# Kernel tuning notes

Hardware: AMD Instinct MI355X
Metric: run time of the kernel (lower is better)

Reference implementation:

```python
import jax, jax.numpy as jnp
import numpy as np

G = 64          # number of global tokens (first G positions are global)
NUM_HEADS = 16
WINDOW = 512    # attention_window (one-sided w = 256)


def _chunk(x, w):
    # x: [BH, S, D] -> overlapping chunks of size 2w with overlap w
    BH, S, D = x.shape
    f = x.reshape(BH, S // w, w, D)
    return jnp.concatenate([f[:, :-1], f[:, 1:]], axis=2)  # [BH, S//w-1, 2w, D]


def _mask_invalid(x, w):
    # x: [B, S, H, 2w+1]; -inf at out-of-sequence window positions
    B, S, H, W = x.shape
    m = jnp.flip(jnp.tril(jnp.ones((w, w + 1), x.dtype)), axis=0)
    m = jnp.pad(m, ((0, S - w), (0, W - w - 1)))
    m = m + jnp.flip(m, axis=(0, 1))
    return jnp.where((m > 0)[None, :, None, :], -jnp.inf, x)


def _sliding_qk(q, k, w):
    # q, k: [B, S, H, D] -> banded scores [B, S, H, 2w+1]
    B, S, H, D = q.shape
    C = S // w - 1
    qf = q.transpose(0, 2, 1, 3).reshape(B * H, S, D)
    kf = k.transpose(0, 2, 1, 3).reshape(B * H, S, D)
    s = jnp.einsum('bcxd,bcyd->bcxy', _chunk(qf, w), _chunk(kf, w))  # [BH,C,2w,2w]
    diag = jnp.pad(s, ((0, 0), (0, 0), (0, 1), (0, 0))).transpose(0, 1, 3, 2)  # [BH,C,2w,2w+1]
    up = jnp.concatenate([diag[:, :, :w, :w + 1], diag[:, -1:, w:, :w + 1]], axis=1)
    z = jnp.zeros((B * H, 1, w, w), diag.dtype)
    low = jnp.concatenate([z, diag[:, :, -(w + 1):-1, w + 1:]], axis=1)
    first = jnp.concatenate([jnp.roll(diag, shift=(1, w), axis=(2, 3))[:, :, :w, :w], z], axis=1)
    low = jnp.where(jnp.arange(C + 1)[None, :, None, None] < 1, first, low)
    full = jnp.concatenate([low, up], axis=-1).reshape(B, H, S, 2 * w + 1).transpose(0, 2, 1, 3)
    return _mask_invalid(full, w)


def _sliding_pv(probs, v, w):
    # probs: [B, S, H, 2w+1], v: [B, S, H, D] -> [B, S, H, D]
    B, S, H, _ = probs.shape
    D = v.shape[-1]
    nc = S // w
    p = probs.transpose(0, 2, 1, 3).reshape(B * H, nc, w, 2 * w + 1)
    vf = v.transpose(0, 2, 1, 3).reshape(B * H, S, D)
    pv = jnp.pad(vf, ((0, 0), (w, w), (0, 0)), constant_values=-1.0)
    idx = jnp.arange(nc)[:, None] * w + jnp.arange(3 * w)[None, :]
    cv = pv[:, idx]  # [BH, nc, 3w, D]
    # pad-and-diagonalize the banded probs into [w, 3w]
    pd = jnp.pad(p, ((0, 0), (0, 0), (0, 0), (0, w + 1)))
    pd = pd.reshape(B * H, nc, w * (3 * w + 2))[:, :, :-w]
    pd = pd.reshape(B * H, nc, w, 3 * w + 1)[:, :, :, :-1]  # [BH,nc,w,3w]
    out = jnp.einsum('bcwd,bcdh->bcwh', pd, cv)
    return out.reshape(B, H, S, D).transpose(0, 2, 1, 3)


def _forward(hidden_states, attention_mask, Wq, bq, Wk, bk, Wv, bv,
             Wqg, bqg, Wkg, bkg, Wvg, bvg, is_index_masked, is_index_global_attn):
    B, S, E = hidden_states.shape
    H = NUM_HEADS
    D = E // H
    w = WINDOW // 2
    q = (hidden_states @ Wq + bq) / jnp.sqrt(jnp.float32(D))
    k = hidden_states @ Wk + bk
    v = hidden_states @ Wv + bv
    q4 = q.reshape(B, S, H, D)
    k4 = k.reshape(B, S, H, D)
    v4 = v.reshape(B, S, H, D)
    local = _sliding_qk(q4, k4, w)                         # [B,S,H,2w+1]
    diag_mask = _sliding_qk(jnp.ones_like(attention_mask), attention_mask, w)  # [B,S,1,2w+1]
    local = local + diag_mask
    # global key columns (first G tokens global) prepended to the band
    g_scores = jnp.einsum('bshd,bghd->bshg', q4, k4[:, :G])
    scores = jnp.concatenate([g_scores, local], axis=-1)   # [B,S,H,G+2w+1]
    probs = jax.nn.softmax(scores, axis=-1)
    probs = jnp.where(is_index_masked[:, :, None, None], 0.0, probs)
    out_g = jnp.einsum('bshg,bghd->bshd', probs[..., :G], v4[:, :G])
    out_l = _sliding_pv(probs[..., G:], v4, w)
    attn_output = (out_g + out_l).reshape(B, S, E)
    # global tokens attend to the full sequence with the *_global projections
    qg = ((hidden_states[:, :G] @ Wqg + bqg) / jnp.sqrt(jnp.float32(D))).reshape(B, G, H, D).transpose(0, 2, 1, 3)
    kg = (hidden_states @ Wkg + bkg).reshape(B, S, H, D).transpose(0, 2, 1, 3)
    vg = (hidden_states @ Wvg + bvg).reshape(B, S, H, D).transpose(0, 2, 1, 3)
    gs = jnp.einsum('bhgd,bhsd->bhgs', qg, kg)             # [B,H,G,S]
    gs = jnp.where(is_index_masked[:, None, None, :], -10000.0, gs)
    gp = jax.nn.softmax(gs, axis=-1)
    go = jnp.einsum('bhgs,bhsd->bhgd', gp, vg).transpose(0, 2, 1, 3).reshape(B, G, E)
    attn_output = attn_output.at[:, :G].set(go)            # scatter global rows
    probs = jnp.where(is_index_global_attn[:, :, None, None], 0.0, probs)
    return attn_output, probs, gp


def setup_inputs() -> dict:
    key = jax.random.key(0)
    B, S, E = 2, 4096, 1024
    ks = jax.random.split(key, 8)
    std = 0.02
    d = lambda k: std * jax.random.normal(k, (E, E), jnp.float32)
    zb = jnp.zeros((E,), jnp.float32)
    return {
        'hidden_states': jax.random.normal(ks[0], (B, S, E), jnp.float32),
        'attention_mask': jnp.zeros((B, S, 1, 1), jnp.float32),
        'Wq': d(ks[1]), 'bq': zb, 'Wk': d(ks[2]), 'bk': zb, 'Wv': d(ks[3]), 'bv': zb,
        'Wqg': d(ks[4]), 'bqg': zb, 'Wkg': d(ks[5]), 'bkg': zb, 'Wvg': d(ks[6]), 'bvg': zb,
        'is_index_masked': jnp.zeros((B, S), bool),
        'is_index_global_attn': jnp.broadcast_to(jnp.arange(S)[None, :] < G, (B, S)),
        'is_global_attn': 1,
    }


def reference(hidden_states, attention_mask, Wq, bq, Wk, bk, Wv, bv,
              Wqg, bqg, Wkg, bkg, Wvg, bvg,
              is_index_masked, is_index_global_attn, is_global_attn):
    # is_global_attn is statically 1 (global path always taken)
    return _forward(hidden_states, attention_mask, Wq, bq, Wk, bk, Wv, bv,
                    Wqg, bqg, Wkg, bkg, Wvg, bvg, is_index_masked, is_index_global_attn)
```

## Files before the change

### kernel.cpp

```cpp
#include <hip/hip_runtime.h>
#include <hip/hip_bf16.h>
#include <cstdint>
#include <cstddef>

typedef short s16x8 __attribute__((ext_vector_type(8)));
typedef float f32x4 __attribute__((ext_vector_type(4)));

#define DEV static __device__ __forceinline__

DEV unsigned short f2bf(float x){
  union { float f; unsigned int u; } v; v.f = x;
  unsigned int u = v.u;
  return (unsigned short)((u + 0x7FFFu + ((u >> 16) & 1u)) >> 16);
}
DEV float bf2f(unsigned short b){
  union { unsigned int u; float f; } v; v.u = ((unsigned int)b) << 16;
  return v.f;
}

DEV void gld16(unsigned short* lds, const unsigned short* g){
  __builtin_amdgcn_global_load_lds(
      (const __attribute__((address_space(1))) void*)g,
      (__attribute__((address_space(3))) void*)lds, 16, 0, 0);
}

__global__ __launch_bounds__(256) void cast_x(const float* __restrict__ X,
                                              unsigned short* __restrict__ out){
  int i = (blockIdx.x*256 + threadIdx.x)*4;
  float4 v = *(const float4*)(X + i);
  ushort4 r;
  r.x = f2bf(v.x); r.y = f2bf(v.y); r.z = f2bf(v.z); r.w = f2bf(v.w);
  *(ushort4*)(out + i) = r;
}

__global__ __launch_bounds__(256) void xg_gather(const float* __restrict__ X,
                                                 unsigned short* __restrict__ Xg){
  int idx = blockIdx.x*256 + threadIdx.x;
  int row = idx >> 10, c = idx & 1023;
  int b = row >> 6, g = row & 63;
  Xg[idx] = f2bf(X[(size_t)(b*4096 + g)*1024 + c]);
}

__global__ __launch_bounds__(256) void bias_cat_k(
    const float* bq, const float* bk, const float* bv,
    const float* bkg, const float* bvg, const float* bqg,
    float* __restrict__ bc, float* __restrict__ bqg_o){
  int i = blockIdx.x*256 + threadIdx.x;
  if (i < 5120){
    int slot = i >> 10, c = i & 1023;
    const float* s = (slot==0)?bq:(slot==1)?bk:(slot==2)?bv:(slot==3)?bkg:bvg;
    bc[i] = s[c];
  } else {
    bqg_o[i-5120] = bqg[i-5120];
  }
}

struct WSrc { const float* p[6]; };

__global__ __launch_bounds__(256) void wt_transpose(WSrc srcs,
    unsigned short* __restrict__ Wtcat, unsigned short* __restrict__ Wtqg){
  __shared__ float t[64*66];
  int bi = blockIdx.x;
  int widx = bi >> 8;
  int tile = bi & 255;
  int tn = tile & 15, tk = tile >> 4;
  int k0 = tk*64, n0 = tn*64;
  const float* W = srcs.p[widx];
  int tid = threadIdx.x;
  for (int it=0; it<8; ++it){
    int flat = it*256 + tid;
    int r = flat >> 5, ch = flat & 31;
    *(float2*)&t[r*66 + ch*2] = *(const float2*)(W + (size_t)(k0+r)*1024 + n0 + ch*2);
  }
  __syncthreads();
  unsigned short* dst = (widx==3) ? Wtqg
                      : Wtcat + (size_t)((widx<3)?widx:widx-1)*1048576;
  for (int it=0; it<16; ++it){
    int flat = it*256 + tid;
    int i = flat >> 6, j = flat & 63;
    dst[(size_t)(n0+i)*1024 + k0 + j] = f2bf(t[j*66 + i]);
  }
}

__global__ __launch_bounds__(256) void gemm_bt(
    const unsigned short* __restrict__ A, const unsigned short* __restrict__ Bt,
    const float* __restrict__ bias, unsigned short* __restrict__ C,
    int Astr, int Bstr, int Cstr, int scale_cols)
{
  __shared__ unsigned short lA[128*64];
  __shared__ unsigned short lB[128*64];
  int tid = threadIdx.x, lane = tid & 63, wv = tid >> 6;
  int wm = wv >> 1, wn = wv & 1;
  int lane15 = lane & 15, kh = (lane >> 4) << 3;
  int m0 = blockIdx.y*128, n0 = blockIdx.x*128;
  f32x4 acc[4][4];
  for (int i=0;i<4;i++) for (int j=0;j<4;j++) acc[i][j] = (f32x4){0.f,0.f,0.f,0.f};
  for (int k0 = 0; k0 < 1024; k0 += 64){
#pragma unroll
    for (int it = 0; it < 4; ++it){
      int chunk = it*256 + tid;
      int r = chunk >> 3, ch = chunk & 7;
      int co = ((ch ^ (r & 7)) << 3);
      gld16(&lA[chunk*8], A  + (size_t)(m0+r)*Astr + k0 + co);
      gld16(&lB[chunk*8], Bt + (size_t)(n0+r)*Bstr + k0 + co);
    }
    __syncthreads();
#pragma unroll
    for (int ks = 0; ks < 2; ++ks){
      s16x8 af[4], bfr[4];
#pragma unroll
      for (int i=0;i<4;i++){
        int row = wm*64 + i*16 + lane15;
        af[i] = *(const s16x8*)&lA[(row<<6) + ((ks*32 + kh) ^ ((row&7)<<3))];
      }
#pragma unroll
      for (int j=0;j<4;j++){
        int row = wn*64 + j*16 + lane15;
        bfr[j] = *(const s16x8*)&lB[(row<<6) + ((ks*32 + kh) ^ ((row&7)<<3))];
      }
#pragma unroll
      for (int i=0;i<4;i++)
#pragma unroll
        for (int j=0;j<4;j++)
          acc[i][j] = __builtin_amdgcn_mfma_f32_16x16x32_bf16(af[i], bfr[j], acc[i][j], 0,0,0);
    }
    __syncthreads();
  }
  for (int i=0;i<4;i++){
    int mb = m0 + wm*64 + i*16 + ((lane>>4)<<2);
    for (int j=0;j<4;j++){
      int n = n0 + wn*64 + j*16 + lane15;
      float bb = bias[n];
      float sc = (n < scale_cols) ? 0.125f : 1.0f;
#pragma unroll
      for (int r=0;r<4;r++)
        C[(size_t)(mb+r)*Cstr + n] = f2bf((acc[i][j][r] + bb)*sc);
    }
  }
}

__global__ __launch_bounds__(256) void vt_transpose(
    const unsigned short* __restrict__ proj, unsigned short* __restrict__ dst,
    int coloff){
  __shared__ unsigned short t[64*72];
  int bi = blockIdx.x;
  int sc = bi & 63, h = (bi>>6) & 15, b = bi >> 10;
  int s0 = sc*64;
  int tid = threadIdx.x;
  for (int it=0; it<2; ++it){
    int flat = it*256 + tid;
    int r = flat >> 3, ch = flat & 7;
    *(int4*)&t[r*72 + ch*8] =
      *(const int4*)(proj + (size_t)(b*4096+s0+r)*5120 + coloff + h*64 + ch*8);
  }
  __syncthreads();
  for (int it=0; it<2; ++it){
    int flat = it*256 + tid;
    int d = flat & 63, ch = flat >> 6;
    unsigned short tmp[8];
#pragma unroll
    for (int j=0;j<8;j++) tmp[j] = t[(ch*8+j)*72 + d];
    *(int4*)(dst + ((size_t)(b*16+h)*64 + d)*4096 + s0 + ch*8) = *(int4*)tmp;
  }
}

#define SSTR 612
__global__ __launch_bounds__(512) void sliding_attn(
    const unsigned short* __restrict__ proj,
    const unsigned short* __restrict__ vt,
    const float* __restrict__ amask,
    const unsigned char* __restrict__ maskb,
    float* __restrict__ probs,
    float* __restrict__ attn)
{
  __shared__ float sS[16*SSTR];
  __shared__ float srs[16];
  int bi = (blockIdx.x & 7)*1024 + (blockIdx.x >> 3);
  int ti = bi & 255, h = (bi>>8) & 15, b = bi >> 12;
  int t = ti*16;
  int chk = t >> 8;
  int qu = (chk < 15) ? chk*256 : 3584;
  int ql = (chk >= 1) ? chk*256 : 256;
  int tid = threadIdx.x, lane = tid & 63, wv = tid >> 6;
  int lane15 = lane & 15, kh = (lane >> 4) << 3;
  int rbase = (lane>>4)<<2;

  s16x8 aq0 = {}, aq1 = {}, ak0a = {}, ak0b = {}, ak1a = {}, ak1b = {};
  {
    int qrow = t + lane15;
    if (wv == 0){
      const unsigned short* qp = proj + (size_t)(b*4096+qrow)*5120 + h*64 + kh;
      aq0 = *(const s16x8*)qp;  aq1 = *(const s16x8*)(qp + 32);
    }
    if (wv >= 4){
      const unsigned short* kp0 = proj + (size_t)(b*4096+qrow)*5120 + 1024 + h*64 + kh;
      ak0a = *(const s16x8*)kp0; ak0b = *(const s16x8*)(kp0 + 32);
    }
    if (wv <= 3){
      int krow = t - 1 + lane15; if (krow < 0) krow = 0;
      const unsigned short* kp1 = proj + (size_t)(b*4096+krow)*5120 + 1024 + h*64 + kh;
      ak1a = *(const s16x8*)kp1; ak1b = *(const s16x8*)(kp1 + 32);
    }
  }

  {
    int ct0 = wv*5;
#pragma unroll
    for (int b2 = 0; b2 < 2; ++b2){
      const int nb = b2 ? 2 : 3;
      int cbase = ct0 + (b2 ? 3 : 0);
      s16x8 B0[3], B1[3];
#pragma unroll
      for (int j = 0; j < nb; ++j){
        int ct = cbase + j;
        if (ct < 37){
          int col = ct*16 + lane15;
          int brow, roff;
          if (ct < 4){        brow = col;               roff = 1024; }
          else if (ct < 20){  brow = ql + 1 + col - 64; roff = 0;
                              if (brow > 4095) brow = 4095; }
          else {              brow = qu + col - 320;    roff = 0; }
          const unsigned short* bp = proj + (size_t)(b*4096+brow)*5120 + roff + h*64 + kh;
          B0[j] = *(const s16x8*)bp;
          B1[j] = *(const s16x8*)(bp + 32);
        }
      }
#pragma unroll
      for (int j = 0; j < nb; ++j){
        int ct = cbase + j;
        if (ct < 37){
          s16x8 A0 = (ct<4) ? aq0 : (ct<20) ? ak1a : ak0a;
          s16x8 A1 = (ct<4) ? aq1 : (ct<20) ? ak1b : ak0b;
          f32x4 acc = (f32x4){0.f,0.f,0.f,0.f};
          acc = __builtin_amdgcn_mfma_f32_16x16x32_bf16(A0, B0[j], acc, 0,0,0);
          acc = __builtin_amdgcn_mfma_f32_16x16x32_bf16(A1, B1[j], acc, 0,0,0);
          int col = ct*16 + lane15;
          if (col <= 576){
            int sk = (ct >= 4);
#pragma unroll
            for (int r=0;r<4;r++){
              int row = rbase + r;
              sS[row*SSTR + col + (sk ? row : 0)] = acc[r];
            }
          }
        }
      }
    }
  }
  __syncthreads();

  {
    int r0 = wv*2;
    float low_add[2], up_add[2];
#pragma unroll
    for (int rr=0;rr<2;rr++){
      int s = t + r0 + rr;
      low_add[rr] = (s >= 1) ? amask[b*4096 + s - 1] : 0.f;
      up_add[rr]  = amask[b*4096 + s];
    }
    float ereg[2][10];
    float m4[2] = {-1e30f,-1e30f};
#pragma unroll
    for (int i=0;i<10;i++){
      int c = lane + i*64;
      bool inr = (c < 577);
      bool isup = (c >= 320), islow = (c >= 64) & !isup;
      int jup = c - 320, jlow = c - 64;
#pragma unroll
      for (int rr=0;rr<2;rr++){
        int r = r0 + rr;
        float v = -1e30f;
        if (inr){
          v = sS[r*SSTR + c + ((c>=64) ? r : 0)];
          int ii = (t + r) & 255;
          if (isup){
            bool valid = !((chk==15) & (jup >= 256 - ii));
            v = valid ? v + up_add[rr] : -1e30f;
          } else if (islow){
            bool valid = !((chk==0) & (jlow < 256 - ii));
            v = valid ? ((jlow==255) ? 0.f : v + low_add[rr]) : -1e30f;
          }
        }
        ereg[rr][i] = v;
        m4[rr] = fmaxf(m4[rr], v);
      }
    }
#pragma unroll
    for (int o=32;o;o>>=1){
#pragma unroll
      for (int rr=0;rr<2;rr++) m4[rr] = fmaxf(m4[rr], __shfl_xor(m4[rr], o));
    }
    float sum4[2] = {0.f,0.f};
#pragma unroll
    for (int i=0;i<10;i++){
      int c = lane + i*64;
      if (c < 577){
#pragma unroll
        for (int rr=0;rr<2;rr++){
          int r = r0 + rr;
          float e = __expf(ereg[rr][i] - m4[rr]);
          ereg[rr][i] = e;
          sum4[rr] += e;
          ((unsigned short*)&sS[r*SSTR])[c + ((c>=64) ? r : 0)] = f2bf(e);
        }
      }
    }
#pragma unroll
    for (int o=32;o;o>>=1){
#pragma unroll
      for (int rr=0;rr<2;rr++) sum4[rr] += __shfl_xor(sum4[rr], o);
    }
#pragma unroll
    for (int rr=0;rr<2;rr++){
      int r = r0 + rr, s = t + r;
      float rs = 1.f / sum4[rr];
      float mz = maskb[b*4096 + s] ? 0.f : 1.f;
      float pz = (s < 64) ? 0.f : mz;
      float* prow = probs + ((size_t)(b*4096+s)*16 + h)*577;
#pragma unroll
      for (int i=0;i<10;i++){
        int c = lane + i*64;
        if (c < 577) prow[c] = ereg[rr][i] * rs * pz;
      }
      if (lane < 31){
        int zc = (lane < r) ? 64 + lane : 577 + lane;
        ((unsigned short*)&sS[r*SSTR])[zc] = 0;
      }
      if (lane == 0) srs[r] = rs * mz;
    }
  }
  __syncthreads();

  int dg = wv & 3, khalf = wv >> 2;
  int dcol = dg*16 + lane15;
  const unsigned short* vtb = vt + ((size_t)(b*16+h)*64 + dcol)*4096;
  const unsigned short* prow16 = (const unsigned short*)(sS + (size_t)lane15*SSTR);
  f32x4 oacc = (f32x4){0.f,0.f,0.f,0.f};
  int kc0 = khalf*10, kcend = kc0 + (khalf ? 9 : 10);
#pragma unroll
  for (int b2 = 0; b2 < 2; ++b2){
    int base = kc0 + b2*5;
    s16x8 vB[5];
#pragma unroll
    for (int j = 0; j < 5; ++j){
      int kc = base + j;
      if (kc < kcend){
        int kk = kc*32 + kh;
        int key = (kk < 64) ? kk : (t - 320 + kk);
        key = key < 0 ? 0 : (key > 4088 ? 4088 : key);
        vB[j] = *(const s16x8*)(vtb + key);
      }
    }
#pragma unroll
    for (int j = 0; j < 5; ++j){
      int kc = base + j;
      if (kc < kcend){
        s16x8 ap = *(const s16x8*)(prow16 + kc*32 + kh);
        oacc = __builtin_amdgcn_mfma_f32_16x16x32_bf16(ap, vB[j], oacc, 0,0,0);
      }
    }
  }
  if (khalf == 1){
#pragma unroll
    for (int r=0;r<4;r++){
      int flat = dg*256 + (rbase + r)*16 + lane15;
      sS[(flat>>8)*SSTR + 336 + (flat & 255)] = oacc[r];
    }
  }
  __syncthreads();
  if (khalf == 0){
#pragma unroll
    for (int r=0;r<4;r++){
      int flat = dg*256 + (rbase + r)*16 + lane15;
      float part = sS[(flat>>8)*SSTR + 336 + (flat & 255)];
      attn[(size_t)(b*4096 + t + rbase + r)*1024 + h*64 + dcol] =
          (oacc[r] + part) * srs[rbase + r];
    }
  }
}

__global__ __launch_bounds__(256) void gs_a2(
    const unsigned short* __restrict__ qg,
    const unsigned short* __restrict__ proj,
    const unsigned char* __restrict__ maskb,
    float* __restrict__ gp)
{
  __shared__ unsigned short sQ[64*68];
  int bi = blockIdx.x;
  int sc = bi & 15, h = (bi>>4) & 15, b = bi >> 8;
  int tid = threadIdx.x, lane = tid & 63, wv = tid >> 6;
  int lane15 = lane & 15, kh = (lane >> 4) << 3;
#pragma unroll
  for (int it=0; it<2; ++it){
    int flat = it*256 + tid;
    int g = flat >> 3, ch = (flat & 7) << 3;
    *(s16x8*)&sQ[g*68 + ch] = *(const s16x8*)(qg + (size_t)(b*64+g)*1024 + h*64 + ch);
  }
  __syncthreads();
  s16x8 a[4][2];
#pragma unroll
  for (int gt=0; gt<4; ++gt)
#pragma unroll
    for (int ks=0; ks<2; ++ks)
      a[gt][ks] = *(const s16x8*)&sQ[(gt*16+lane15)*68 + ks*32 + kh];
  int s0 = sc*256 + wv*64;
  float* gpb_ = gp + (size_t)(b*16+h)*64*4096;
#pragma unroll
  for (int st=0; st<4; ++st){
    int s = s0 + st*16 + lane15;
    const unsigned short* kp = proj + (size_t)(b*4096+s)*5120 + 3072 + h*64 + kh;
    s16x8 b0 = *(const s16x8*)kp;
    s16x8 b1 = *(const s16x8*)(kp + 32);
    bool msk = maskb[b*4096 + s] != 0;
    f32x4 acc[4];
#pragma unroll
    for (int gt=0; gt<4; ++gt){
      acc[gt] = (f32x4){0.f,0.f,0.f,0.f};
      acc[gt] = __builtin_amdgcn_mfma_f32_16x16x32_bf16(a[gt][0], b0, acc[gt], 0,0,0);
      acc[gt] = __builtin_amdgcn_mfma_f32_16x16x32_bf16(a[gt][1], b1, acc[gt], 0,0,0);
    }
#pragma unroll
    for (int gt=0; gt<4; ++gt){
#pragma unroll
      for (int r=0;r<4;r++){
        int g = gt*16 + (lane>>4)*4 + r;
        gpb_[(size_t)g*4096 + s] = msk ? -10000.f : acc[gt][r];
      }
    }
  }
}

__global__ __launch_bounds__(256) void gs_norm(float* __restrict__ gp,
                                               unsigned short* __restrict__ gpb){
  __shared__ float red[8];
  int bi = blockIdx.x;
  float* row = gp + (size_t)bi*4096;
  int tid = threadIdx.x, lane = tid & 63, wv = tid >> 6;
  float v[16];
  float m = -1e30f;
#pragma unroll
  for (int i=0;i<16;i++){
    v[i] = row[tid + i*256];
    m = fmaxf(m, v[i]);
  }
#pragma unroll
  for (int o=32;o;o>>=1) m = fmaxf(m, __shfl_xor(m, o));
  if (!lane) red[wv] = m;
  __syncthreads();
  m = fmaxf(fmaxf(red[0],red[1]), fmaxf(red[2],red[3]));
  float s = 0.f;
#pragma unroll
  for (int i=0;i<16;i++){
    float e = __expf(v[i] - m);
    v[i] = e;
    s += e;
  }
#pragma unroll
  for (int o=32;o;o>>=1) s += __shfl_xor(s, o);
  if (!lane) red[4+wv] = s;
  __syncthreads();
  s = red[4]+red[5]+red[6]+red[7];
  float rs = 1.f / s;
#pragma unroll
  for (int i=0;i<16;i++){
    float p = v[i] * rs;
    row[tid + i*256] = p;
    gpb[(size_t)bi*4096 + tid + i*256] = f2bf(p);
  }
}

__global__ __launch_bounds__(256) void go_mfma(
    const unsigned short* __restrict__ gpb,
    const unsigned short* __restrict__ vgt,
    float* __restrict__ gop)
{
  int bi = blockIdx.x;
  int kc = bi & 7, bh = bi >> 3;
  int tid = threadIdx.x, lane = tid & 63, wv = tid >> 6;
  int lane15 = lane & 15, kh = (lane >> 4) << 3;
  const unsigned short* arow = gpb + ((size_t)bh*64 + wv*16 + lane15)*4096 + kh;
  const unsigned short* bbase = vgt + (size_t)bh*64*4096 + kh;
  f32x4 acc[4];
#pragma unroll
  for (int j=0;j<4;j++) acc[j] = (f32x4){0.f,0.f,0.f,0.f};
  for (int ks = 0; ks < 16; ++ks){
    int k = kc*512 + ks*32;
    s16x8 a = *(const s16x8*)(arow + k);
#pragma unroll
    for (int j=0;j<4;j++){
      s16x8 bv = *(const s16x8*)(bbase + (size_t)(j*16 + lane15)*4096 + k);
      acc[j] = __builtin_amdgcn_mfma_f32_16x16x32_bf16(a, bv, acc[j], 0,0,0);
    }
  }
  int rq = (lane >> 4) << 2;
  float* o = gop + ((size_t)bh*8 + kc)*4096;
#pragma unroll
  for (int j=0;j<4;j++)
#pragma unroll
    for (int r=0;r<4;r++)
      o[(wv*16 + rq + r)*64 + j*16 + lane15] = acc[j][r];
}

__global__ __launch_bounds__(256) void reduce_go2(
    const float* __restrict__ gop, float* __restrict__ attn){
  int flat = blockIdx.x*256 + threadIdx.x;
  int gd = flat & 4095, bh = flat >> 12;
  int b = bh >> 4, h = bh & 15;
  int g = gd >> 6, d = gd & 63;
  const float* p = gop + (size_t)bh*8*4096 + gd;
  float sum = 0.f;
#pragma unroll
  for (int c=0; c<8; ++c) sum += p[c*4096];
  attn[(size_t)(b*4096 + g)*1024 + h*64 + d] = sum;
}

extern "C" void kernel_launch(void* const* d_in, const int* in_sizes, int n_in,
                              void* d_out, int out_size, void* d_ws, size_t ws_size,
                              hipStream_t stream)
{
  const float* X     = (const float*)d_in[0];
  const float* amask = (const float*)d_in[1];
  const float* Wq  = (const float*)d_in[2];  const float* bq  = (const float*)d_in[3];
  const float* Wk  = (const float*)d_in[4];  const float* bk  = (const float*)d_in[5];
  const float* Wv  = (const float*)d_in[6];  const float* bv  = (const float*)d_in[7];
  const float* Wqg = (const float*)d_in[8];  const float* bqg = (const float*)d_in[9];
  const float* Wkg = (const float*)d_in[10]; const float* bkg = (const float*)d_in[11];
  const float* Wvg = (const float*)d_in[12]; const float* bvg = (const float*)d_in[13];
  const unsigned char* imask = (const unsigned char*)d_in[14];
  (void)in_sizes; (void)n_in; (void)out_size;

  const size_t XBF  = 0;
  const size_t XG   = 16777216;
  const size_t WT   = 17039360;
  const size_t WTQG = 27525120;
  const size_t BC   = 29622272;
  const size_t BQG  = 29642752;
  const size_t PROJ = 29646848;
  const size_t QGO  = 113532928;
  const size_t VT   = 113795072;
  const size_t NEED = 130572288;
  if (ws_size < NEED) return;

  char* ws = (char*)d_ws;
  unsigned short* Xbf   = (unsigned short*)(ws + XBF);
  unsigned short* Xg    = (unsigned short*)(ws + XG);
  unsigned short* Wtcat = (unsigned short*)(ws + WT);
  unsigned short* Wtqg  = (unsigned short*)(ws + WTQG);
  float*          bc    = (float*)(ws + BC);
  float*          bqgo  = (float*)(ws + BQG);
  unsigned short* proj  = (unsigned short*)(ws + PROJ);
  unsigned short* qgo   = (unsigned short*)(ws + QGO);
  unsigned short* vt    = (unsigned short*)(ws + VT);
  unsigned short* gpb   = (unsigned short*)(ws + XBF);
  float*          gop   = (float*)(ws + WT);

  float* attn  = (float*)d_out;
  float* probs = (float*)d_out + 8388608;
  float* gp    = (float*)d_out + 84017152;

  cast_x<<<8192, 256, 0, stream>>>(X, Xbf);
  xg_gather<<<512, 256, 0, stream>>>(X, Xg);
  bias_cat_k<<<24, 256, 0, stream>>>(bq, bk, bv, bkg, bvg, bqg, bc, bqgo);
  WSrc srcs; srcs.p[0]=Wq; srcs.p[1]=Wk; srcs.p[2]=Wv; srcs.p[3]=Wqg; srcs.p[4]=Wkg; srcs.p[5]=Wvg;
  wt_transpose<<<1536, 256, 0, stream>>>(srcs, Wtcat, Wtqg);
  gemm_bt<<<dim3(40,64), 256, 0, stream>>>(Xbf, Wtcat, bc, proj, 1024, 1024, 5120, 1024);
  gemm_bt<<<dim3(8,1),  256, 0, stream>>>(Xg, Wtqg, bqgo, qgo, 1024, 1024, 1024, 1024);
  vt_transpose<<<2048, 256, 0, stream>>>(proj, vt, 2048);
  sliding_attn<<<8192, 512, 0, stream>>>(proj, vt, amask, imask, probs, attn);
  vt_transpose<<<2048, 256, 0, stream>>>(proj, vt, 4096);
  gs_a2<<<512, 256, 0, stream>>>(qgo, proj, imask, gp);
  gs_norm<<<2048, 256, 0, stream>>>(gp, gpb);
  go_mfma<<<256, 256, 0, stream>>>(gpb, vt, gop);
  reduce_go2<<<512, 256, 0, stream>>>(gop, attn);
}
```

Before: 421.1 us.

## Stage shared Q windows in LDS and process four query tiles per block

Each sliding_attn block now handles four consecutive 16-row query tiles of the same chunk and head instead of one, launching a quarter as many blocks. The 256-row lower and upper Q windows for the chunk are loaded once into a swizzled dynamic LDS buffer via global_load_lds and reused across the four tiles. This replaces repeated global loads of the B operand for the QK scores. In exchange the block uses about 100KB of LDS, which cuts occupancy to one block per CU, and adds a barrier per tile iteration.

```diff
diff --git a/kernel.cpp b/kernel.cpp
--- a/kernel.cpp
+++ b/kernel.cpp
@@ -165,6 +165,7 @@
 }
 
 #define SSTR 612
+#define SLDS_BYTES 104768
 __global__ __launch_bounds__(512) void sliding_attn(
     const unsigned short* __restrict__ proj,
     const unsigned short* __restrict__ vt,
@@ -173,68 +174,87 @@
     float* __restrict__ probs,
     float* __restrict__ attn)
 {
-  __shared__ float sS[16*SSTR];
-  __shared__ float srs[16];
-  int bi = (blockIdx.x & 7)*1024 + (blockIdx.x >> 3);
-  int ti = bi & 255, h = (bi>>8) & 15, b = bi >> 12;
-  int t = ti*16;
-  int chk = t >> 8;
+  extern __shared__ char smem[];
+  float* sS = (float*)smem;
+  float* srs = (float*)(smem + 39168);
+  unsigned short* loP = (unsigned short*)(smem + 39232);
+  unsigned short* upP = (unsigned short*)(smem + 72000);
+
+  int blk = blockIdx.x;
+  int bi = (blk & 7)*256 + (blk >> 3);
+  int quad = bi & 3, c = (bi>>2) & 15, h = (bi>>6) & 15, b = bi >> 10;
+  int chk = c;
   int qu = (chk < 15) ? chk*256 : 3584;
   int ql = (chk >= 1) ? chk*256 : 256;
   int tid = threadIdx.x, lane = tid & 63, wv = tid >> 6;
   int lane15 = lane & 15, kh = (lane >> 4) << 3;
   int rbase = (lane>>4)<<2;
 
-  s16x8 aq0 = {}, aq1 = {}, ak0a = {}, ak0b = {}, ak1a = {}, ak1b = {};
-  {
-    int qrow = t + lane15;
-    if (wv == 0){
-      const unsigned short* qp = proj + (size_t)(b*4096+qrow)*5120 + h*64 + kh;
-      aq0 = *(const s16x8*)qp;  aq1 = *(const s16x8*)(qp + 32);
-    }
-    if (wv >= 4){
-      const unsigned short* kp0 = proj + (size_t)(b*4096+qrow)*5120 + 1024 + h*64 + kh;
-      ak0a = *(const s16x8*)kp0; ak0b = *(const s16x8*)(kp0 + 32);
-    }
-    if (wv <= 3){
-      int krow = t - 1 + lane15; if (krow < 0) krow = 0;
-      const unsigned short* kp1 = proj + (size_t)(b*4096+krow)*5120 + 1024 + h*64 + kh;
-      ak1a = *(const s16x8*)kp1; ak1b = *(const s16x8*)(kp1 + 32);
-    }
-  }
-
-  {
-    int ct0 = wv*5;
-#pragma unroll
-    for (int b2 = 0; b2 < 2; ++b2){
-      const int nb = b2 ? 2 : 3;
-      int cbase = ct0 + (b2 ? 3 : 0);
-      s16x8 B0[3], B1[3];
-#pragma unroll
-      for (int j = 0; j < nb; ++j){
-        int ct = cbase + j;
+#pragma unroll
+  for (int it=0; it<4; ++it){
+    int cidx = it*512 + tid, r = cidx>>3, ch = cidx&7;
+    int lrow = ql + 1 + r; if (lrow > 4095) lrow = 4095;
+    gld16(&loP[cidx*8], proj + (size_t)(b*4096+lrow)*5120 + h*64 + ((ch ^ (r&7))<<3));
+  }
+#pragma unroll
+  for (int it=0; it<4; ++it){
+    int cidx = it*512 + tid, r = cidx>>3, ch = cidx&7;
+    gld16(&upP[cidx*8], proj + (size_t)(b*4096+qu+r)*5120 + h*64 + ((ch ^ (r&7))<<3));
+  }
+  __syncthreads();
+
+  for (int tt = 0; tt < 4; ++tt){
+    int t = (c*16 + quad*4 + tt)*16;
+
+    s16x8 aq0 = {}, aq1 = {}, ak0a = {}, ak0b = {}, ak1a = {}, ak1b = {};
+    {
+      int qrow = t + lane15;
+      if (wv == 0){
+        const unsigned short* qp = proj + (size_t)(b*4096+qrow)*5120 + h*64 + kh;
+        aq0 = *(const s16x8*)qp;  aq1 = *(const s16x8*)(qp + 32);
+      }
+      if (wv >= 4){
+        const unsigned short* kp0 = proj + (size_t)(b*4096+qrow)*5120 + 1024 + h*64 + kh;
+        ak0a = *(const s16x8*)kp0; ak0b = *(const s16x8*)(kp0 + 32);
+      }
+      if (wv <= 3){
+        int krow = t - 1 + lane15; if (krow < 0) krow = 0;
+        const unsigned short* kp1 = proj + (size_t)(b*4096+krow)*5120 + 1024 + h*64 + kh;
+        ak1a = *(const s16x8*)kp1; ak1b = *(const s16x8*)(kp1 + 32);
+      }
+    }
+
+    {
+      int ct0 = wv*5;
+#pragma unroll
+      for (int j5 = 0; j5 < 5; ++j5){
+        int ct = ct0 + j5;
         if (ct < 37){
           int col = ct*16 + lane15;
-          int brow, roff;
-          if (ct < 4){        brow = col;               roff = 1024; }
-          else if (ct < 20){  brow = ql + 1 + col - 64; roff = 0;
-                              if (brow > 4095) brow = 4095; }
-          else {              brow = qu + col - 320;    roff = 0; }
-          const unsigned short* bp = proj + (size_t)(b*4096+brow)*5120 + roff + h*64 + kh;
-          B0[j] = *(const s16x8*)bp;
-          B1[j] = *(const s16x8*)(bp + 32);
-        }
-      }
-#pragma unroll
-      for (int j = 0; j < nb; ++j){
-        int ct = cbase + j;
-        if (ct < 37){
+          s16x8 B0, B1;
+          if (ct < 4){
+            const unsigned short* bp = proj + (size_t)(b*4096+col)*5120 + 1024 + h*64 + kh;
+            B0 = *(const s16x8*)bp; B1 = *(const s16x8*)(bp + 32);
+          } else if (ct == 36){
+            int brow = qu + col - 320; if (brow > 4095) brow = 4095;
+            const unsigned short* bp = proj + (size_t)(b*4096+brow)*5120 + h*64 + kh;
+            B0 = *(const s16x8*)bp; B1 = *(const s16x8*)(bp + 32);
+          } else if (ct < 20){
+            int j2 = col - 64;
+            const unsigned short* pp = loP + j2*64;
+            B0 = *(const s16x8*)(pp + (kh ^ ((j2&7)<<3)));
+            B1 = *(const s16x8*)(pp + ((32+kh) ^ ((j2&7)<<3)));
+          } else {
+            int j2 = col - 320;
+            const unsigned short* pp = upP + j2*64;
+            B0 = *(const s16x8*)(pp + (kh ^ ((j2&7)<<3)));
+            B1 = *(const s16x8*)(pp + ((32+kh) ^ ((j2&7)<<3)));
+          }
           s16x8 A0 = (ct<4) ? aq0 : (ct<20) ? ak1a : ak0a;
           s16x8 A1 = (ct<4) ? aq1 : (ct<20) ? ak1b : ak0b;
           f32x4 acc = (f32x4){0.f,0.f,0.f,0.f};
-          acc = __builtin_amdgcn_mfma_f32_16x16x32_bf16(A0, B0[j], acc, 0,0,0);
-          acc = __builtin_amdgcn_mfma_f32_16x16x32_bf16(A1, B1[j], acc, 0,0,0);
-          int col = ct*16 + lane15;
+          acc = __builtin_amdgcn_mfma_f32_16x16x32_bf16(A0, B0, acc, 0,0,0);
+          acc = __builtin_amdgcn_mfma_f32_16x16x32_bf16(A1, B1, acc, 0,0,0);
           if (col <= 576){
             int sk = (ct >= 4);
 #pragma unroll
@@ -246,136 +266,137 @@
         }
       }
     }
-  }
-  __syncthreads();
-
-  {
-    int r0 = wv*2;
-    float low_add[2], up_add[2];
-#pragma unroll
-    for (int rr=0;rr<2;rr++){
-      int s = t + r0 + rr;
-      low_add[rr] = (s >= 1) ? amask[b*4096 + s - 1] : 0.f;
-      up_add[rr]  = amask[b*4096 + s];
-    }
-    float ereg[2][10];
-    float m4[2] = {-1e30f,-1e30f};
-#pragma unroll
-    for (int i=0;i<10;i++){
-      int c = lane + i*64;
-      bool inr = (c < 577);
-      bool isup = (c >= 320), islow = (c >= 64) & !isup;
-      int jup = c - 320, jlow = c - 64;
+    __syncthreads();
+
+    {
+      int r0 = wv*2;
+      float low_add[2], up_add[2];
 #pragma unroll
       for (int rr=0;rr<2;rr++){
-        int r = r0 + rr;
-        float v = -1e30f;
-        if (inr){
-          v = sS[r*SSTR + c + ((c>=64) ? r : 0)];
-          int ii = (t + r) & 255;
-          if (isup){
-            bool valid = !((chk==15) & (jup >= 256 - ii));
-            v = valid ? v + up_add[rr] : -1e30f;
-          } else if (islow){
-            bool valid = !((chk==0) & (jlow < 256 - ii));
-            v = valid ? ((jlow==255) ? 0.f : v + low_add[rr]) : -1e30f;
-          }
-        }
-        ereg[rr][i] = v;
-        m4[rr] = fmaxf(m4[rr], v);
-      }
-    }
-#pragma unroll
-    for (int o=32;o;o>>=1){
-#pragma unroll
-      for (int rr=0;rr<2;rr++) m4[rr] = fmaxf(m4[rr], __shfl_xor(m4[rr], o));
-    }
-    float sum4[2] = {0.f,0.f};
-#pragma unroll
-    for (int i=0;i<10;i++){
-      int c = lane + i*64;
-      if (c < 577){
+        int s = t + r0 + rr;
+        low_add[rr] = (s >= 1) ? amask[b*4096 + s - 1] : 0.f;
+        up_add[rr]  = amask[b*4096 + s];
+      }
+      float ereg[2][10];
+      float m4[2] = {-1e30f,-1e30f};
+#pragma unroll
+      for (int i=0;i<10;i++){
+        int cc = lane + i*64;
+        bool inr = (cc < 577);
+        bool isup = (cc >= 320), islow = (cc >= 64) & !isup;
+        int jup = cc - 320, jlow = cc - 64;
 #pragma unroll
         for (int rr=0;rr<2;rr++){
           int r = r0 + rr;
-          float e = __expf(ereg[rr][i] - m4[rr]);
-          ereg[rr][i] = e;
-          sum4[rr] += e;
-          ((unsigned short*)&sS[r*SSTR])[c + ((c>=64) ? r : 0)] = f2bf(e);
-        }
-      }
-    }
-#pragma unroll
-    for (int o=32;o;o>>=1){
-#pragma unroll
-      for (int rr=0;rr<2;rr++) sum4[rr] += __shfl_xor(sum4[rr], o);
-    }
-#pragma unroll
-    for (int rr=0;rr<2;rr++){
-      int r = r0 + rr, s = t + r;
-      float rs = 1.f / sum4[rr];
-      float mz = maskb[b*4096 + s] ? 0.f : 1.f;
-      float pz = (s < 64) ? 0.f : mz;
-      float* prow = probs + ((size_t)(b*4096+s)*16 + h)*577;
+          float v = -1e30f;
+          if (inr){
+            v = sS[r*SSTR + cc + ((cc>=64) ? r : 0)];
+            int ii = (t + r) & 255;
+            if (isup){
+              bool valid = !((chk==15) & (jup >= 256 - ii));
+              v = valid ? v + up_add[rr] : -1e30f;
+            } else if (islow){
+              bool valid = !((chk==0) & (jlow < 256 - ii));
+              v = valid ? ((jlow==255) ? 0.f : v + low_add[rr]) : -1e30f;
+            }
+          }
+          ereg[rr][i] = v;
+          m4[rr] = fmaxf(m4[rr], v);
+        }
+      }
+#pragma unroll
+      for (int o=32;o;o>>=1){
+#pragma unroll
+        for (int rr=0;rr<2;rr++) m4[rr] = fmaxf(m4[rr], __shfl_xor(m4[rr], o));
+      }
+      float sum4[2] = {0.f,0.f};
 #pragma unroll
       for (int i=0;i<10;i++){
-        int c = lane + i*64;
-        if (c < 577) prow[c] = ereg[rr][i] * rs * pz;
-      }
-      if (lane < 31){
-        int zc = (lane < r) ? 64 + lane : 577 + lane;
-        ((unsigned short*)&sS[r*SSTR])[zc] = 0;
-      }
-      if (lane == 0) srs[r] = rs * mz;
-    }
-  }
-  __syncthreads();
-
-  int dg = wv & 3, khalf = wv >> 2;
-  int dcol = dg*16 + lane15;
-  const unsigned short* vtb = vt + ((size_t)(b*16+h)*64 + dcol)*4096;
-  const unsigned short* prow16 = (const unsigned short*)(sS + (size_t)lane15*SSTR);
-  f32x4 oacc = (f32x4){0.f,0.f,0.f,0.f};
-  int kc0 = khalf*10, kcend = kc0 + (khalf ? 9 : 10);
-#pragma unroll
-  for (int b2 = 0; b2 < 2; ++b2){
-    int base = kc0 + b2*5;
-    s16x8 vB[5];
-#pragma unroll
-    for (int j = 0; j < 5; ++j){
-      int kc = base + j;
-      if (kc < kcend){
-        int kk = kc*32 + kh;
-        int key = (kk < 64) ? kk : (t - 320 + kk);
-        key = key < 0 ? 0 : (key > 4088 ? 4088 : key);
-        vB[j] = *(const s16x8*)(vtb + key);
-      }
-    }
-#pragma unroll
-    for (int j = 0; j < 5; ++j){
-      int kc = base + j;
-      if (kc < kcend){
-        s16x8 ap = *(const s16x8*)(prow16 + kc*32 + kh);
-        oacc = __builtin_amdgcn_mfma_f32_16x16x32_bf16(ap, vB[j], oacc, 0,0,0);
-      }
-    }
-  }
-  if (khalf == 1){
-#pragma unroll
-    for (int r=0;r<4;r++){
-      int flat = dg*256 + (rbase + r)*16 + lane15;
-      sS[(flat>>8)*SSTR + 336 + (flat & 255)] = oacc[r];
-    }
-  }
-  __syncthreads();
-  if (khalf == 0){
-#pragma unroll
-    for (int r=0;r<4;r++){
-      int flat = dg*256 + (rbase + r)*16 + lane15;
-      float part = sS[(flat>>8)*SSTR + 336 + (flat & 255)];
-      attn[(size_t)(b*4096 + t + rbase + r)*1024 + h*64 + dcol] =
-          (oacc[r] + part) * srs[rbase + r];
-    }
+        int cc = lane + i*64;
+        if (cc < 577){
+#pragma unroll
+          for (int rr=0;rr<2;rr++){
+            int r = r0 + rr;
+            float e = __expf(ereg[rr][i] - m4[rr]);
+            ereg[rr][i] = e;
+            sum4[rr] += e;
+            ((unsigned short*)&sS[r*SSTR])[cc + ((cc>=64) ? r : 0)] = f2bf(e);
+          }
+        }
+      }
+#pragma unroll
+      for (int o=32;o;o>>=1){
+#pragma unroll
+        for (int rr=0;rr<2;rr++) sum4[rr] += __shfl_xor(sum4[rr], o);
+      }
+#pragma unroll
+      for (int rr=0;rr<2;rr++){
+        int r = r0 + rr, s = t + r;
+        float rs = 1.f / sum4[rr];
+        float mz = maskb[b*4096 + s] ? 0.f : 1.f;
+        float pz = (s < 64) ? 0.f : mz;
+        float* prow = probs + ((size_t)(b*4096+s)*16 + h)*577;
+#pragma unroll
+        for (int i=0;i<10;i++){
+          int cc = lane + i*64;
+          if (cc < 577) prow[cc] = ereg[rr][i] * rs * pz;
+        }
+        if (lane < 31){
+          int zc = (lane < r) ? 64 + lane : 577 + lane;
+          ((unsigned short*)&sS[r*SSTR])[zc] = 0;
+        }
+        if (lane == 0) srs[r] = rs * mz;
+      }
+    }
+    __syncthreads();
+
+    int dg = wv & 3, khalf = wv >> 2;
+    int dcol = dg*16 + lane15;
+    const unsigned short* vtb = vt + ((size_t)(b*16+h)*64 + dcol)*4096;
+    const unsigned short* prow16 = (const unsigned short*)(sS + (size_t)lane15*SSTR);
+    f32x4 oacc = (f32x4){0.f,0.f,0.f,0.f};
+    int kc0 = khalf*10, kcend = kc0 + (khalf ? 9 : 10);
+#pragma unroll
+    for (int b2 = 0; b2 < 2; ++b2){
+      int base = kc0 + b2*5;
+      s16x8 vB[5];
+#pragma unroll
+      for (int j = 0; j < 5; ++j){
+        int kc = base + j;
+        if (kc < kcend){
+          int kk = kc*32 + kh;
+          int key = (kk < 64) ? kk : (t - 320 + kk);
+          key = key < 0 ? 0 : (key > 4088 ? 4088 : key);
+          vB[j] = *(const s16x8*)(vtb + key);
+        }
+      }
+#pragma unroll
+      for (int j = 0; j < 5; ++j){
+        int kc = base + j;
+        if (kc < kcend){
+          s16x8 ap = *(const s16x8*)(prow16 + kc*32 + kh);
+          oacc = __builtin_amdgcn_mfma_f32_16x16x32_bf16(ap, vB[j], oacc, 0,0,0);
+        }
+      }
+    }
+    if (khalf == 1){
+#pragma unroll
+      for (int r=0;r<4;r++){
+        int flat = dg*256 + (rbase + r)*16 + lane15;
+        sS[(flat>>8)*SSTR + 336 + (flat & 255)] = oacc[r];
+      }
+    }
+    __syncthreads();
+    if (khalf == 0){
+#pragma unroll
+      for (int r=0;r<4;r++){
+        int flat = dg*256 + (rbase + r)*16 + lane15;
+        float part = sS[(flat>>8)*SSTR + 336 + (flat & 255)];
+        attn[(size_t)(b*4096 + t + rbase + r)*1024 + h*64 + dcol] =
+            (oacc[r] + part) * srs[rbase + r];
+      }
+    }
+    __syncthreads();
   }
 }
 
@@ -558,6 +579,9 @@
   float* probs = (float*)d_out + 8388608;
   float* gp    = (float*)d_out + 84017152;
 
+  hipFuncSetAttribute((const void*)sliding_attn,
+                      hipFuncAttributeMaxDynamicSharedMemorySize, SLDS_BYTES);
+
   cast_x<<<8192, 256, 0, stream>>>(X, Xbf);
   xg_gather<<<512, 256, 0, stream>>>(X, Xg);
   bias_cat_k<<<24, 256, 0, stream>>>(bq, bk, bv, bkg, bvg, bqg, bc, bqgo);
@@ -566,7 +590,7 @@
   gemm_bt<<<dim3(40,64), 256, 0, stream>>>(Xbf, Wtcat, bc, proj, 1024, 1024, 5120, 1024);
   gemm_bt<<<dim3(8,1),  256, 0, stream>>>(Xg, Wtqg, bqgo, qgo, 1024, 1024, 1024, 1024);
   vt_transpose<<<2048, 256, 0, stream>>>(proj, vt, 2048);
-  sliding_attn<<<8192, 512, 0, stream>>>(proj, vt, amask, imask, probs, attn);
+  sliding_attn<<<2048, 512, SLDS_BYTES, stream>>>(proj, vt, amask, imask, probs, attn);
   vt_transpose<<<2048, 256, 0, stream>>>(proj, vt, 4096);
   gs_a2<<<512, 256, 0, stream>>>(qgo, proj, imask, gp);
   gs_norm<<<2048, 256, 0, stream>>>(gp, gpb);
```

New measurement: 468.9 us. 1.11x slower.

## Split sliding attention into separate QK-softmax and PV kernels

Applied to the files above, without the earlier changes.

The fused sliding-window kernel is split in two. The first kernel computes the banded scores and softmax and writes fp32 probs. A new 256-thread PV kernel re-reads those probs from global memory, converts them to bf16 into LDS and runs the MFMA against V. The QK loop also drops its batched B-operand loads, and an explicit lgkmcnt barrier replaces __syncthreads. The aim is lower LDS and register pressure per kernel and a simpler PV reduction, at the cost of an extra full read of the large fp32 probs tensor. The PV output now takes its scaling and masking from the stored probs, so rows where those probs are zeroed (the first 64 global-token rows and masked rows) change behaviour unless later kernels overwrite them.

```diff
diff --git a/kernel.cpp b/kernel.cpp
--- a/kernel.cpp
+++ b/kernel.cpp
@@ -16,6 +16,12 @@
 DEV float bf2f(unsigned short b){
   union { unsigned int u; float f; } v; v.u = ((unsigned int)b) << 16;
   return v.f;
+}
+
+DEV void bar_lgkm(){
+  asm volatile("s_waitcnt lgkmcnt(0)" ::: "memory");
+  __builtin_amdgcn_s_barrier();
+  __builtin_amdgcn_sched_barrier(0);
 }
 
 DEV void gld16(unsigned short* lds, const unsigned short* g){
@@ -165,16 +171,13 @@
 }
 
 #define SSTR 612
-__global__ __launch_bounds__(512) void sliding_attn(
+__global__ __launch_bounds__(512) void sliding_qk(
     const unsigned short* __restrict__ proj,
-    const unsigned short* __restrict__ vt,
     const float* __restrict__ amask,
     const unsigned char* __restrict__ maskb,
-    float* __restrict__ probs,
-    float* __restrict__ attn)
+    float* __restrict__ probs)
 {
   __shared__ float sS[16*SSTR];
-  __shared__ float srs[16];
   int bi = (blockIdx.x & 7)*1024 + (blockIdx.x >> 3);
   int ti = bi & 255, h = (bi>>8) & 15, b = bi >> 12;
   int t = ti*16;
@@ -206,48 +209,35 @@
   {
     int ct0 = wv*5;
 #pragma unroll
-    for (int b2 = 0; b2 < 2; ++b2){
-      const int nb = b2 ? 2 : 3;
-      int cbase = ct0 + (b2 ? 3 : 0);
-      s16x8 B0[3], B1[3];
-#pragma unroll
-      for (int j = 0; j < nb; ++j){
-        int ct = cbase + j;
-        if (ct < 37){
-          int col = ct*16 + lane15;
-          int brow, roff;
-          if (ct < 4){        brow = col;               roff = 1024; }
-          else if (ct < 20){  brow = ql + 1 + col - 64; roff = 0;
-                              if (brow > 4095) brow = 4095; }
-          else {              brow = qu + col - 320;    roff = 0; }
-          const unsigned short* bp = proj + (size_t)(b*4096+brow)*5120 + roff + h*64 + kh;
-          B0[j] = *(const s16x8*)bp;
-          B1[j] = *(const s16x8*)(bp + 32);
-        }
-      }
-#pragma unroll
-      for (int j = 0; j < nb; ++j){
-        int ct = cbase + j;
-        if (ct < 37){
-          s16x8 A0 = (ct<4) ? aq0 : (ct<20) ? ak1a : ak0a;
-          s16x8 A1 = (ct<4) ? aq1 : (ct<20) ? ak1b : ak0b;
-          f32x4 acc = (f32x4){0.f,0.f,0.f,0.f};
-          acc = __builtin_amdgcn_mfma_f32_16x16x32_bf16(A0, B0[j], acc, 0,0,0);
-          acc = __builtin_amdgcn_mfma_f32_16x16x32_bf16(A1, B1[j], acc, 0,0,0);
-          int col = ct*16 + lane15;
-          if (col <= 576){
-            int sk = (ct >= 4);
-#pragma unroll
-            for (int r=0;r<4;r++){
-              int row = rbase + r;
-              sS[row*SSTR + col + (sk ? row : 0)] = acc[r];
-            }
+    for (int j5 = 0; j5 < 5; ++j5){
+      int ct = ct0 + j5;
+      if (ct < 37){
+        int col = ct*16 + lane15;
+        int brow, roff;
+        if (ct < 4){        brow = col;               roff = 1024; }
+        else if (ct < 20){  brow = ql + 1 + col - 64; roff = 0;
+                            if (brow > 4095) brow = 4095; }
+        else {              brow = qu + col - 320;    roff = 0; }
+        const unsigned short* bp = proj + (size_t)(b*4096+brow)*5120 + roff + h*64 + kh;
+        s16x8 b0 = *(const s16x8*)bp;
+        s16x8 b1 = *(const s16x8*)(bp + 32);
+        s16x8 A0 = (ct<4) ? aq0 : (ct<20) ? ak1a : ak0a;
+        s16x8 A1 = (ct<4) ? aq1 : (ct<20) ? ak1b : ak0b;
+        f32x4 acc = (f32x4){0.f,0.f,0.f,0.f};
+        acc = __builtin_amdgcn_mfma_f32_16x16x32_bf16(A0, b0, acc, 0,0,0);
+        acc = __builtin_amdgcn_mfma_f32_16x16x32_bf16(A1, b1, acc, 0,0,0);
+        if (col <= 576){
+          int sk = (ct >= 4);
+#pragma unroll
+          for (int r=0;r<4;r++){
+            int row = rbase + r;
+            sS[row*SSTR + col + (sk ? row : 0)] = acc[r];
           }
         }
       }
     }
   }
-  __syncthreads();
+  bar_lgkm();
 
   {
     int r0 = wv*2;
@@ -297,11 +287,9 @@
       if (c < 577){
 #pragma unroll
         for (int rr=0;rr<2;rr++){
-          int r = r0 + rr;
           float e = __expf(ereg[rr][i] - m4[rr]);
           ereg[rr][i] = e;
           sum4[rr] += e;
-          ((unsigned short*)&sS[r*SSTR])[c + ((c>=64) ? r : 0)] = f2bf(e);
         }
       }
     }
@@ -322,29 +310,50 @@
         int c = lane + i*64;
         if (c < 577) prow[c] = ereg[rr][i] * rs * pz;
       }
-      if (lane < 31){
-        int zc = (lane < r) ? 64 + lane : 577 + lane;
-        ((unsigned short*)&sS[r*SSTR])[zc] = 0;
-      }
-      if (lane == 0) srs[r] = rs * mz;
-    }
-  }
-  __syncthreads();
-
-  int dg = wv & 3, khalf = wv >> 2;
-  int dcol = dg*16 + lane15;
+    }
+  }
+}
+
+#define PSTR2 648
+__global__ __launch_bounds__(256) void sliding_pv(
+    const float* __restrict__ probs,
+    const unsigned short* __restrict__ vt,
+    float* __restrict__ attn)
+{
+  __shared__ unsigned short sPe[16*PSTR2];
+  int bi = (blockIdx.x & 7)*1024 + (blockIdx.x >> 3);
+  int ti = bi & 255, h = (bi>>8) & 15, b = bi >> 12;
+  int t = ti*16;
+  int tid = threadIdx.x, lane = tid & 63, wv = tid >> 6;
+  int lane15 = lane & 15, kh = (lane >> 4) << 3;
+  int rbase = (lane>>4)<<2;
+
+  for (int i = tid; i < 16*608; i += 256){
+    int row = i / 608, scol = i - row*608;
+    const float* prow = probs + ((size_t)(b*4096 + t + row)*16 + h)*577;
+    float v;
+    if (scol < 64){
+      v = prow[scol];
+    } else {
+      int c = scol - row;
+      v = (c >= 64 && c < 577) ? prow[c] : 0.f;
+    }
+    sPe[row*PSTR2 + scol] = f2bf(v);
+  }
+  bar_lgkm();
+
+  int dcol = wv*16 + lane15;
   const unsigned short* vtb = vt + ((size_t)(b*16+h)*64 + dcol)*4096;
-  const unsigned short* prow16 = (const unsigned short*)(sS + (size_t)lane15*SSTR);
+  const unsigned short* prow16 = sPe + (size_t)lane15*PSTR2;
   f32x4 oacc = (f32x4){0.f,0.f,0.f,0.f};
-  int kc0 = khalf*10, kcend = kc0 + (khalf ? 9 : 10);
-#pragma unroll
-  for (int b2 = 0; b2 < 2; ++b2){
-    int base = kc0 + b2*5;
+#pragma unroll
+  for (int b2 = 0; b2 < 4; ++b2){
+    int base = b2*5;
     s16x8 vB[5];
 #pragma unroll
     for (int j = 0; j < 5; ++j){
       int kc = base + j;
-      if (kc < kcend){
+      if (kc < 19){
         int kk = kc*32 + kh;
         int key = (kk < 64) ? kk : (t - 320 + kk);
         key = key < 0 ? 0 : (key > 4088 ? 4088 : key);
@@ -354,29 +363,15 @@
 #pragma unroll
     for (int j = 0; j < 5; ++j){
       int kc = base + j;
-      if (kc < kcend){
+      if (kc < 19){
         s16x8 ap = *(const s16x8*)(prow16 + kc*32 + kh);
         oacc = __builtin_amdgcn_mfma_f32_16x16x32_bf16(ap, vB[j], oacc, 0,0,0);
       }
     }
   }
-  if (khalf == 1){
-#pragma unroll
-    for (int r=0;r<4;r++){
-      int flat = dg*256 + (rbase + r)*16 + lane15;
-      sS[(flat>>8)*SSTR + 336 + (flat & 255)] = oacc[r];
-    }
-  }
-  __syncthreads();
-  if (khalf == 0){
-#pragma unroll
-    for (int r=0;r<4;r++){
-      int flat = dg*256 + (rbase + r)*16 + lane15;
-      float part = sS[(flat>>8)*SSTR + 336 + (flat & 255)];
-      attn[(size_t)(b*4096 + t + rbase + r)*1024 + h*64 + dcol] =
-          (oacc[r] + part) * srs[rbase + r];
-    }
-  }
+#pragma unroll
+  for (int r=0;r<4;r++)
+    attn[(size_t)(b*4096 + t + rbase + r)*1024 + h*64 + dcol] = oacc[r];
 }
 
 __global__ __launch_bounds__(256) void gs_a2(
@@ -566,7 +561,8 @@
   gemm_bt<<<dim3(40,64), 256, 0, stream>>>(Xbf, Wtcat, bc, proj, 1024, 1024, 5120, 1024);
   gemm_bt<<<dim3(8,1),  256, 0, stream>>>(Xg, Wtqg, bqgo, qgo, 1024, 1024, 1024, 1024);
   vt_transpose<<<2048, 256, 0, stream>>>(proj, vt, 2048);
-  sliding_attn<<<8192, 512, 0, stream>>>(proj, vt, amask, imask, probs, attn);
+  sliding_qk<<<8192, 512, 0, stream>>>(proj, amask, imask, probs);
+  sliding_pv<<<8192, 256, 0, stream>>>(probs, vt, attn);
   vt_transpose<<<2048, 256, 0, stream>>>(proj, vt, 4096);
   gs_a2<<<512, 256, 0, stream>>>(qgo, proj, imask, gp);
   gs_norm<<<2048, 256, 0, stream>>>(gp, gpb);
```

Measured after the change: 526.5 us. 25.0% more time.
